# Kernel optimization log

Hardware: AMD Instinct MI355X
Metric: run time of the kernel (lower is better)

## Reference

```python
import jax, jax.numpy as jnp
import numpy as np

B, L, H, C = 1, 512, 1024, 2


def setup_inputs() -> dict:
    key = jax.random.key(0)
    k1, k2, k3 = jax.random.split(key, 3)
    lm_output = jax.random.normal(k1, (B, L, H), dtype=jnp.float32)
    # torch Linear weight layout: [out_features, in_features]
    W1 = jax.random.normal(k2, (H, 2 * H), dtype=jnp.float32) * 0.02
    b1 = jnp.zeros((H,), dtype=jnp.float32)
    W2 = jax.random.normal(k3, (C, H), dtype=jnp.float32) * 0.02
    b2 = jnp.zeros((C,), dtype=jnp.float32)
    return {"lm_output": lm_output, "W1": W1, "b1": b1, "W2": W2, "b2": b2}


def reference(lm_output, W1, b1, W2, b2):
    # pair_emb[b,i,j] = concat(lm_output[b,j], lm_output[b,i])
    # Linear(concat(a,b)) decomposes: split W1 into the halves acting on each part.
    Wa = W1[:, :H]  # acts on lm_output_a (the j / column token)
    Wb = W1[:, H:]  # acts on lm_output_b (the i / row token)
    a_proj = jnp.einsum('blh,oh->blo', lm_output, Wa)  # [B,L,H]
    b_proj = jnp.einsum('blh,oh->blo', lm_output, Wb)  # [B,L,H]
    # hidden[b,i,j] = tanh(a_proj[b,j] + b_proj[b,i] + b1)   -> [B,L,L,H]
    hidden = jnp.tanh(a_proj[:, None, :, :] + b_proj[:, :, None, :] + b1)
    # Dropout is identity at inference time.
    logits = jnp.einsum('bijh,ch->bijc', hidden, W2) + b2  # [B,L,L,C]
    logits = (logits + jnp.swapaxes(logits, 1, 2)) / 2.0
    return logits
```

## Files before the change

### kernel.cpp

```cpp
#include <hip/hip_runtime.h>
#include <hip/hip_bf16.h>

#define HH 1024
#define LL 512
#define NT 16
#define NTRI 136
#define NZ 8

typedef __attribute__((ext_vector_type(8))) short bf16x8;
typedef __attribute__((ext_vector_type(4))) float f32x4;
typedef __attribute__((ext_vector_type(2))) float f32x2;

static constexpr float C_EXP = 2.8853900817779268f;

static __device__ __forceinline__ uint4 pack8(float4 a, float4 b) {
    union { uint4 u; __hip_bfloat162 h[4]; } r;
    r.h[0] = __float22bfloat162_rn(make_float2(a.x, a.y));
    r.h[1] = __float22bfloat162_rn(make_float2(a.z, a.w));
    r.h[2] = __float22bfloat162_rn(make_float2(b.x, b.y));
    r.h[3] = __float22bfloat162_rn(make_float2(b.z, b.w));
    return r.u;
}

__global__ __launch_bounds__(256, 4) void proj_mfma_kernel(
    const float* __restrict__ lm, const float* __restrict__ W1,
    const float* __restrict__ b1, float* __restrict__ Ea, float* __restrict__ Eb)
{
    __shared__ ushort As[64][136];
    __shared__ ushort Bs[32][136];

    const int tid  = threadIdx.x;
    const int lane = tid & 63;
    const int w    = tid >> 6;
    const int b    = blockIdx.x;
    const int xcd  = b & 7;
    const int idx  = b >> 3;
    const int nbase = (xcd * 8 + (idx & 7)) * 32;
    const int mbase = (idx >> 3) * 64;
    const int wm   = w * 16;
    const int sel  = nbase >> 10;
    const int nrow = nbase & 1023;

    const int frow = lane & 15;
    const int q8   = (lane >> 4) * 8;

    f32x4 acc[2] = {};

    for (int kb = 0; kb < HH; kb += 128) {
        __syncthreads();
        {
            int p = tid;
#pragma unroll
            for (int it = 0; it < 4; ++it, p += 256) {
                const int row = p >> 4, c8 = (p & 15) * 8;
                const float* pa = &lm[(mbase + row) * HH + kb + c8];
                *(uint4*)&As[row][c8] = pack8(*(const float4*)pa, *(const float4*)(pa + 4));
            }
            int q = tid;
#pragma unroll
            for (int it = 0; it < 2; ++it, q += 256) {
                const int row = q >> 4, c8 = (q & 15) * 8;
                const float* pw = &W1[(nrow + row) * 2048 + sel * 1024 + kb + c8];
                *(uint4*)&Bs[row][c8] = pack8(*(const float4*)pw, *(const float4*)(pw + 4));
            }
        }
        __syncthreads();

#pragma unroll
        for (int s = 0; s < 4; ++s) {
            const bf16x8 a = *(const bf16x8*)&As[wm + frow][s * 32 + q8];
#pragma unroll
            for (int nf = 0; nf < 2; ++nf) {
                const bf16x8 bb = *(const bf16x8*)&Bs[nf * 16 + frow][s * 32 + q8];
                acc[nf] = __builtin_amdgcn_mfma_f32_16x16x32_bf16(a, bb, acc[nf], 0, 0, 0);
            }
        }
    }

    const int col = lane & 15;
    const int rq  = (lane >> 4) * 4;
    const int m0  = mbase + wm + rq;
    const bool isA = sel == 0;
#pragma unroll
    for (int nf = 0; nf < 2; ++nf) {
        const int nn = (nrow + nf * 16 + col);
        if (isA) {
            const float bb = b1[nn];
#pragma unroll
            for (int r = 0; r < 4; ++r)
                Ea[(m0 + r) * HH + nn] = __builtin_amdgcn_exp2f(C_EXP * (acc[nf][r] + bb));
        } else {
#pragma unroll
            for (int r = 0; r < 4; ++r)
                Eb[(m0 + r) * HH + nn] = __builtin_amdgcn_exp2f(C_EXP * acc[nf][r]);
        }
    }
}

__global__ __launch_bounds__(256, 5) void pair_kernel(
    const float* __restrict__ Ea, const float* __restrict__ Eb,
    const float* __restrict__ W2, float* __restrict__ pbuf, int slice)
{
    __shared__ float tl[4][32][64];

    const int tid = threadIdx.x;
    const int tx  = tid & 15;
    const int ty  = tid >> 4;

    int tt = blockIdx.x, bi = 0, rem = NT;
    while (tt >= rem) { tt -= rem; --rem; ++bi; }
    const int bj    = bi + tt;
    const int ibase = bi * 32;
    const int jbase = bj * 32;
    const int k0    = blockIdx.y * slice;

    f32x2 aC0[2] = {}, aC1[2] = {};
    const f32x2 one2 = {1.f, 1.f};

    float4 st[8];

#define LOADS(hh)                                                              \
    {                                                                          \
        int p = tid;                                                           \
        _Pragma("unroll")                                                      \
        for (int it = 0; it < 8; ++it, p += 256) {                             \
            const int tile = p >> 9;                                           \
            const int row  = (p >> 4) & 31;                                    \
            const int c4   = p & 15;                                           \
            if      (tile == 0) st[it] = *(const float4*)&Ea[(jbase + row) * HH + (hh) + c4 * 4]; \
            else if (tile == 1) st[it] = *(const float4*)&Ea[(ibase + row) * HH + (hh) + c4 * 4]; \
            else if (tile == 2) st[it] = *(const float4*)&Eb[(ibase + row) * HH + (hh) + c4 * 4]; \
            else                st[it] = *(const float4*)&Eb[(jbase + row) * HH + (hh) + c4 * 4]; \
        }                                                                      \
    }

#define STORES()                                                               \
    {                                                                          \
        int p = tid;                                                           \
        _Pragma("unroll")                                                      \
        for (int it = 0; it < 8; ++it, p += 256) {                             \
            const int tile = p >> 9;                                           \
            const int row  = (p >> 4) & 31;                                    \
            const int c4   = p & 15;                                           \
            const int c4s  = (tile == 0 || tile == 3) ? (c4 ^ (row & 15)) : c4;\
            *(float4*)&tl[tile][row][c4s * 4] = st[it];                        \
        }                                                                      \
    }

#define COMPUTE(kb)                                                            \
    _Pragma("unroll 4")                                                        \
    for (int h4 = 0; h4 < 16; ++h4) {                                          \
        const int sx = (h4 ^ tx) * 4;                 \
        const float4 Aj0 = *(const float4*)&tl[0][tx][sx];                     \
        const float4 Aj1 = *(const float4*)&tl[0][tx + 16][sx];                \
        const float4 Bj0 = *(const float4*)&tl[3][tx][sx];                     \
        const float4 Bj1 = *(const float4*)&tl[3][tx + 16][sx];                \
        const float4 Ai0 = *(const float4*)&tl[1][ty][h4 * 4];                 \
        const float4 Ai1 = *(const float4*)&tl[1][ty + 16][h4 * 4];            \
        const float4 Bi0 = *(const float4*)&tl[2][ty][h4 * 4];                 \
        const float4 Bi1 = *(const float4*)&tl[2][ty + 16][h4 * 4];            \
        const float4 w0q = *(const float4*)&W2[k0 + (kb) + h4 * 4];            \
        const float4 w1q = *(const float4*)&W2[HH + k0 + (kb) + h4 * 4];       \
        DO_H(Aj0.x, Aj1.x, Bi0.x, Bi1.x, Ai0.x, Ai1.x, Bj0.x, Bj1.x, w0q.x, w1q.x) \
        DO_H(Aj0.y, Aj1.y, Bi0.y, Bi1.y, Ai0.y, Ai1.y, Bj0.y, Bj1.y, w0q.y, w1q.y) \
        DO_H(Aj0.z, Aj1.z, Bi0.z, Bi1.z, Ai0.z, Ai1.z, Bj0.z, Bj1.z, w0q.z, w1q.z) \
        DO_H(Aj0.w, Aj1.w, Bi0.w, Bi1.w, Ai0.w, Ai1.w, Bj0.w, Bj1.w, w0q.w, w1q.w) \
    }

#define DO_H(AJ0v, AJ1v, BI0v, BI1v, AI0v, AI1v, BJ0v, BJ1v, W0s, W1s)        \
    {                                                                          \
        const f32x2 Aj = {AJ0v, AJ1v};                                         \
        const f32x2 Bj = {BJ0v, BJ1v};                                         \
        const f32x2 d0 = __builtin_elementwise_fma((f32x2){BI0v, BI0v}, Aj, one2); \
        const f32x2 d1 = __builtin_elementwise_fma((f32x2){BI1v, BI1v}, Aj, one2); \
        const f32x2 e0 = __builtin_elementwise_fma((f32x2){AI0v, AI0v}, Bj, one2); \
        const f32x2 e1 = __builtin_elementwise_fma((f32x2){AI1v, AI1v}, Bj, one2); \
        const float dp0 = d0.x * d0.y, dp1 = d1.x * d1.y;                      \
        const float ep0 = e0.x * e0.y, ep1 = e1.x * e1.y;                      \
        const float DR = __builtin_amdgcn_rcpf(dp0 * dp1);                     \
        const float ER = __builtin_amdgcn_rcpf(ep0 * ep1);                     \
        const f32x2 dq = (f32x2){DR, DR} * (f32x2){dp1, dp0};                  \
        const f32x2 eq = (f32x2){ER, ER} * (f32x2){ep1, ep0};                  \
        const f32x2 u0 = (f32x2){dq.x, dq.x} * __builtin_shufflevector(d0, d0, 1, 0) \
                       + (f32x2){eq.x, eq.x} * __builtin_shufflevector(e0, e0, 1, 0); \
        const f32x2 u1 = (f32x2){dq.y, dq.y} * __builtin_shufflevector(d1, d1, 1, 0) \
                       + (f32x2){eq.y, eq.y} * __builtin_shufflevector(e1, e1, 1, 0); \
        aC0[0] = __builtin_elementwise_fma(u0, (f32x2){(W0s), (W0s)}, aC0[0]); \
        aC1[0] = __builtin_elementwise_fma(u0, (f32x2){(W1s), (W1s)}, aC1[0]); \
        aC0[1] = __builtin_elementwise_fma(u1, (f32x2){(W0s), (W0s)}, aC0[1]); \
        aC1[1] = __builtin_elementwise_fma(u1, (f32x2){(W1s), (W1s)}, aC1[1]); \
    }

    LOADS(k0);
    STORES();
    for (int kb = 0; kb < slice; kb += 64) {
        const bool more = (kb + 64 < slice);
        if (more) LOADS(k0 + kb + 64);
        __syncthreads();
        COMPUTE(kb)
        if (more) {
            __syncthreads();
            STORES();
        }
    }

#undef DO_H
#undef COMPUTE
#undef STORES
#undef LOADS

    float* pb = pbuf + ((size_t)blockIdx.y * NTRI + blockIdx.x) * 2048;
#pragma unroll
    for (int ii = 0; ii < 2; ++ii)
#pragma unroll
        for (int jj = 0; jj < 2; ++jj) {
            const int li = ty + ii * 16, lj = tx + jj * 16;
            const f32x2 v = { jj ? aC0[ii].y : aC0[ii].x,
                              jj ? aC1[ii].y : aC1[ii].x };
            *(f32x2*)&pb[(li * 32 + lj) * 2] = v;
        }
}

__global__ __launch_bounds__(256) void combine_kernel(
    const float* __restrict__ pbuf, const float* __restrict__ W2,
    const float* __restrict__ b2, float* __restrict__ out, int nz)
{
    __shared__ float s_ws[2];

    const int tid = threadIdx.x;
    if (tid < 128) {
        const int c = tid >> 6, l = tid & 63;
        float s = 0.f;
#pragma unroll
        for (int q = 0; q < 4; ++q) {
            const float4 v = *(const float4*)&W2[c * HH + (l + q * 64) * 4];
            s += v.x + v.y + v.z + v.w;
        }
#pragma unroll
        for (int off = 32; off; off >>= 1) s += __shfl_down(s, off, 64);
        if (l == 0) s_ws[c] = s + b2[c];
    }
    __syncthreads();

    const int idx   = blockIdx.x * 256 + tid;
    const int t     = idx >> 11;
    const int local = idx & 2047;
    int tt = t, bi = 0, rem = NT;
    while (tt >= rem) { tt -= rem; --rem; ++bi; }
    const int bj = bi + tt;

    float s0 = 0.f, s1 = 0.f, s2 = 0.f, s3 = 0.f;
    for (int z = 0; z < nz; z += 4) {
        s0 += pbuf[((size_t)z * NTRI + t) * 2048 + local];
        s1 += pbuf[((size_t)(z + 1) * NTRI + t) * 2048 + local];
        s2 += pbuf[((size_t)(z + 2) * NTRI + t) * 2048 + local];
        s3 += pbuf[((size_t)(z + 3) * NTRI + t) * 2048 + local];
    }
    const float s = (s0 + s1) + (s2 + s3);

    const int li = local >> 6;
    const int lj = (local >> 1) & 31;
    const int c  = local & 1;
    const float v = s_ws[c] - s;

    const int i = bi * 32 + li;
    const int j = bj * 32 + lj;
    out[(i * LL + j) * 2 + c] = v;
    out[(j * LL + i) * 2 + c] = v;
}

extern "C" void kernel_launch(void* const* d_in, const int* in_sizes, int n_in,
                              void* d_out, int out_size, void* d_ws, size_t ws_size,
                              hipStream_t stream)
{
    const float* lm = (const float*)d_in[0];
    const float* W1 = (const float*)d_in[1];
    const float* b1 = (const float*)d_in[2];
    const float* W2 = (const float*)d_in[3];
    const float* b2 = (const float*)d_in[4];
    float* out = (float*)d_out;

    char* ws = (char*)d_ws;
    float* Ea   = (float*)ws;
    float* Eb   = (float*)(ws + (2u << 20));
    float* pbuf = (float*)(ws + (4u << 20) + 64);

    const int nz = NZ;
    const int slice = HH / nz;

    proj_mfma_kernel<<<512, 256, 0, stream>>>(lm, W1, b1, Ea, Eb);
    pair_kernel<<<dim3(NTRI, nz), 256, 0, stream>>>(Ea, Eb, W2, pbuf, slice);
    combine_kernel<<<(NTRI * 2048) / 256, 256, 0, stream>>>(pbuf, W2, b2, out, nz);
}
```

Measured before the change: 139.1 us.

## Stage pair-kernel tiles with direct global-to-LDS loads and double buffering

Replaces the register-staged global→shared copies in pair_kernel with `__builtin_amdgcn_global_load_lds`. Each wave streams one of the four Ea/Eb tiles straight into LDS, and the XOR swizzle moves onto the source address. The hidden-dim chunk shrinks from 64 to 32, with two LDS buffers and a fixed four-phase loop, so the next chunk's load overlaps compute. The goal is to cut VGPR staging pressure and the extra barrier per iteration. In exchange it hardcodes a slice of 128 and lowers the launch_bounds occupancy hint from 5 to 4 blocks.

```diff
diff --git a/kernel.cpp b/kernel.cpp
--- a/kernel.cpp
+++ b/kernel.cpp
@@ -13,7 +13,7 @@
 
 static constexpr float C_EXP = 2.8853900817779268f;
 
-static __device__ __forceinline__ uint4 pack8(float4 a, float4 b) {
+static __device__ __forceinline__ uint4 pack8(f32x4 a, f32x4 b) {
     union { uint4 u; __hip_bfloat162 h[4]; } r;
     r.h[0] = __float22bfloat162_rn(make_float2(a.x, a.y));
     r.h[1] = __float22bfloat162_rn(make_float2(a.z, a.w));
@@ -54,14 +54,14 @@
             for (int it = 0; it < 4; ++it, p += 256) {
                 const int row = p >> 4, c8 = (p & 15) * 8;
                 const float* pa = &lm[(mbase + row) * HH + kb + c8];
-                *(uint4*)&As[row][c8] = pack8(*(const float4*)pa, *(const float4*)(pa + 4));
+                *(uint4*)&As[row][c8] = pack8(*(const f32x4*)pa, *(const f32x4*)(pa + 4));
             }
             int q = tid;
 #pragma unroll
             for (int it = 0; it < 2; ++it, q += 256) {
                 const int row = q >> 4, c8 = (q & 15) * 8;
                 const float* pw = &W1[(nrow + row) * 2048 + sel * 1024 + kb + c8];
-                *(uint4*)&Bs[row][c8] = pack8(*(const float4*)pw, *(const float4*)(pw + 4));
+                *(uint4*)&Bs[row][c8] = pack8(*(const f32x4*)pw, *(const f32x4*)(pw + 4));
             }
         }
         __syncthreads();
@@ -97,11 +97,11 @@
     }
 }
 
-__global__ __launch_bounds__(256, 5) void pair_kernel(
+__global__ __launch_bounds__(256, 4) void pair_kernel(
     const float* __restrict__ Ea, const float* __restrict__ Eb,
     const float* __restrict__ W2, float* __restrict__ pbuf, int slice)
 {
-    __shared__ float tl[4][32][64];
+    __shared__ float tl[2][4][32][32];
 
     const int tid = threadIdx.x;
     const int tx  = tid & 15;
@@ -117,54 +117,24 @@
     f32x2 aC0[2] = {}, aC1[2] = {};
     const f32x2 one2 = {1.f, 1.f};
 
-    float4 st[8];
-
-#define LOADS(hh)                                                              \
+    const int wv = tid >> 6, ln = tid & 63;
+    const int rr = ln >> 3, ss = ln & 7;
+    const float* mat   = (wv <= 1) ? Ea : Eb;
+    const int    rbase = (wv == 0 || wv == 3) ? jbase : ibase;
+    const bool   swz   = (wv == 0 || wv == 3);
+
+#define STAGE(b, kk)                                                           \
     {                                                                          \
-        int p = tid;                                                           \
         _Pragma("unroll")                                                      \
-        for (int it = 0; it < 8; ++it, p += 256) {                             \
-            const int tile = p >> 9;                                           \
-            const int row  = (p >> 4) & 31;                                    \
-            const int c4   = p & 15;                                           \
-            if      (tile == 0) st[it] = *(const float4*)&Ea[(jbase + row) * HH + (hh) + c4 * 4]; \
-            else if (tile == 1) st[it] = *(const float4*)&Ea[(ibase + row) * HH + (hh) + c4 * 4]; \
-            else if (tile == 2) st[it] = *(const float4*)&Eb[(ibase + row) * HH + (hh) + c4 * 4]; \
-            else                st[it] = *(const float4*)&Eb[(jbase + row) * HH + (hh) + c4 * 4]; \
+        for (int k = 0; k < 4; ++k) {                                          \
+            const int row = k * 8 + rr;                                        \
+            const int sc  = swz ? (ss ^ (row & 7)) : ss;                       \
+            const float* g = &mat[(size_t)(rbase + row) * HH + (kk) + sc * 4]; \
+            __builtin_amdgcn_global_load_lds(                                  \
+                (const __attribute__((address_space(1))) unsigned int*)g,      \
+                (__attribute__((address_space(3))) unsigned int*)&tl[b][wv][k * 8][0], \
+                16, 0, 0);                                                     \
         }                                                                      \
-    }
-
-#define STORES()                                                               \
-    {                                                                          \
-        int p = tid;                                                           \
-        _Pragma("unroll")                                                      \
-        for (int it = 0; it < 8; ++it, p += 256) {                             \
-            const int tile = p >> 9;                                           \
-            const int row  = (p >> 4) & 31;                                    \
-            const int c4   = p & 15;                                           \
-            const int c4s  = (tile == 0 || tile == 3) ? (c4 ^ (row & 15)) : c4;\
-            *(float4*)&tl[tile][row][c4s * 4] = st[it];                        \
-        }                                                                      \
-    }
-
-#define COMPUTE(kb)                                                            \
-    _Pragma("unroll 4")                                                        \
-    for (int h4 = 0; h4 < 16; ++h4) {                                          \
-        const int sx = (h4 ^ tx) * 4;                 \
-        const float4 Aj0 = *(const float4*)&tl[0][tx][sx];                     \
-        const float4 Aj1 = *(const float4*)&tl[0][tx + 16][sx];                \
-        const float4 Bj0 = *(const float4*)&tl[3][tx][sx];                     \
-        const float4 Bj1 = *(const float4*)&tl[3][tx + 16][sx];                \
-        const float4 Ai0 = *(const float4*)&tl[1][ty][h4 * 4];                 \
-        const float4 Ai1 = *(const float4*)&tl[1][ty + 16][h4 * 4];            \
-        const float4 Bi0 = *(const float4*)&tl[2][ty][h4 * 4];                 \
-        const float4 Bi1 = *(const float4*)&tl[2][ty + 16][h4 * 4];            \
-        const float4 w0q = *(const float4*)&W2[k0 + (kb) + h4 * 4];            \
-        const float4 w1q = *(const float4*)&W2[HH + k0 + (kb) + h4 * 4];       \
-        DO_H(Aj0.x, Aj1.x, Bi0.x, Bi1.x, Ai0.x, Ai1.x, Bj0.x, Bj1.x, w0q.x, w1q.x) \
-        DO_H(Aj0.y, Aj1.y, Bi0.y, Bi1.y, Ai0.y, Ai1.y, Bj0.y, Bj1.y, w0q.y, w1q.y) \
-        DO_H(Aj0.z, Aj1.z, Bi0.z, Bi1.z, Ai0.z, Ai1.z, Bj0.z, Bj1.z, w0q.z, w1q.z) \
-        DO_H(Aj0.w, Aj1.w, Bi0.w, Bi1.w, Ai0.w, Ai1.w, Bj0.w, Bj1.w, w0q.w, w1q.w) \
     }
 
 #define DO_H(AJ0v, AJ1v, BI0v, BI1v, AI0v, AI1v, BJ0v, BJ1v, W0s, W1s)        \
@@ -191,23 +161,38 @@
         aC1[1] = __builtin_elementwise_fma(u1, (f32x2){(W1s), (W1s)}, aC1[1]); \
     }
 
-    LOADS(k0);
-    STORES();
-    for (int kb = 0; kb < slice; kb += 64) {
-        const bool more = (kb + 64 < slice);
-        if (more) LOADS(k0 + kb + 64);
-        __syncthreads();
-        COMPUTE(kb)
-        if (more) {
-            __syncthreads();
-            STORES();
-        }
-    }
-
+#define COMPUTE(b, kk)                                                         \
+    _Pragma("unroll 4")                                                        \
+    for (int h4 = 0; h4 < 8; ++h4) {                                           \
+        const int sx = (h4 ^ (tx & 7)) * 4;             \
+        const f32x4 Aj0 = *(const f32x4*)&tl[b][0][tx][sx];                    \
+        const f32x4 Aj1 = *(const f32x4*)&tl[b][0][tx + 16][sx];               \
+        const f32x4 Bj0 = *(const f32x4*)&tl[b][3][tx][sx];                    \
+        const f32x4 Bj1 = *(const f32x4*)&tl[b][3][tx + 16][sx];               \
+        const f32x4 Ai0 = *(const f32x4*)&tl[b][1][ty][h4 * 4];                \
+        const f32x4 Ai1 = *(const f32x4*)&tl[b][1][ty + 16][h4 * 4];           \
+        const f32x4 Bi0 = *(const f32x4*)&tl[b][2][ty][h4 * 4];                \
+        const f32x4 Bi1 = *(const f32x4*)&tl[b][2][ty + 16][h4 * 4];           \
+        const f32x4 w0q = *(const f32x4*)&W2[k0 + (kk) + h4 * 4];              \
+        const f32x4 w1q = *(const f32x4*)&W2[HH + k0 + (kk) + h4 * 4];         \
+        DO_H(Aj0.x, Aj1.x, Bi0.x, Bi1.x, Ai0.x, Ai1.x, Bj0.x, Bj1.x, w0q.x, w1q.x) \
+        DO_H(Aj0.y, Aj1.y, Bi0.y, Bi1.y, Ai0.y, Ai1.y, Bj0.y, Bj1.y, w0q.y, w1q.y) \
+        DO_H(Aj0.z, Aj1.z, Bi0.z, Bi1.z, Ai0.z, Ai1.z, Bj0.z, Bj1.z, w0q.z, w1q.z) \
+        DO_H(Aj0.w, Aj1.w, Bi0.w, Bi1.w, Ai0.w, Ai1.w, Bj0.w, Bj1.w, w0q.w, w1q.w) \
+    }
+
+    STAGE(0, k0)
+    __syncthreads();
+#pragma unroll
+    for (int ph = 0; ph < 4; ++ph) {
+        if (ph < 3) STAGE((ph + 1) & 1, k0 + (ph + 1) * 32)
+        COMPUTE(ph & 1, ph * 32)
+        if (ph < 3) __syncthreads();
+    }
+
+#undef COMPUTE
 #undef DO_H
-#undef COMPUTE
-#undef STORES
-#undef LOADS
+#undef STAGE
 
     float* pb = pbuf + ((size_t)blockIdx.y * NTRI + blockIdx.x) * 2048;
 #pragma unroll
@@ -233,7 +218,7 @@
         float s = 0.f;
 #pragma unroll
         for (int q = 0; q < 4; ++q) {
-            const float4 v = *(const float4*)&W2[c * HH + (l + q * 64) * 4];
+            const f32x4 v = *(const f32x4*)&W2[c * HH + (l + q * 64) * 4];
             s += v.x + v.y + v.z + v.w;
         }
 #pragma unroll
```

Result: faster. 128.1 us (-7.9%).
